# Kernel tuning notes

Hardware: AMD Instinct MI355X
Metric: run time of the kernel (lower is better)

## Reference

```python
import jax, jax.numpy as jnp
import numpy as np

EMBED = 2048
HEADS = 16
DHEAD = EMBED // HEADS


def setup_inputs() -> dict:
    key = jax.random.key(0)
    k1, k2, k3 = jax.random.split(key, 3)
    x = jax.random.normal(k1, (4, 2048, EMBED), dtype=jnp.float32)
    # torch Linear weight layout: [out_features, in_features]; y = x @ W.T
    W_in = jax.random.normal(k2, (3 * EMBED, EMBED), dtype=jnp.float32) * (EMBED ** -0.5)
    W_out = jax.random.normal(k3, (EMBED, EMBED), dtype=jnp.float32) * (EMBED ** -0.5)
    return {"x": x, "W_in": W_in, "W_out": W_out}


def reference(x, W_in, W_out):
    B, T, C = x.shape
    qkv = jnp.einsum('btc,fc->btf', x, W_in)          # [B,T,3C]
    q, k, v = jnp.split(qkv, 3, axis=-1)
    def heads(t):
        return t.reshape(B, T, HEADS, DHEAD).transpose(0, 2, 1, 3)  # [B,H,T,D]
    q, k, v = heads(q), heads(k), heads(v)
    scale = DHEAD ** -0.5
    scores = jnp.einsum('bhtd,bhsd->bhts', q, k) * scale  # [B,H,T,T]
    causal = jnp.tril(jnp.ones((T, T), dtype=bool))
    scores = jnp.where(causal, scores, jnp.finfo(scores.dtype).min)
    attn = jax.nn.softmax(scores, axis=-1)
    y = jnp.einsum('bhts,bhsd->bhtd', attn, v)            # [B,H,T,D]
    y = y.transpose(0, 2, 1, 3).reshape(B, T, C)
    return jnp.einsum('btc,fc->btf', y, W_out)
```

## Files before the change

kernel.cpp:

```cpp
#include <hip/hip_runtime.h>

typedef unsigned short u16;
typedef unsigned int u32;
typedef __attribute__((ext_vector_type(8))) short bf16x8;
typedef __attribute__((ext_vector_type(4))) float f32x4;
typedef __attribute__((ext_vector_type(8))) unsigned short u16x8;
typedef __attribute__((ext_vector_type(4))) unsigned short u16x4;
typedef __attribute__((ext_vector_type(4))) u32 u32x4;

#define MFMA16 __builtin_amdgcn_mfma_f32_16x16x32_bf16

__device__ __forceinline__ u16 f2bf(float f) {
  unsigned u = __float_as_uint(f);
  u += 0x7fffu + ((u >> 16) & 1u);
  return (u16)(u >> 16);
}

__device__ __forceinline__ void async16(void* lds, const void* g) {
  __builtin_amdgcn_global_load_lds(
      (const __attribute__((address_space(1))) unsigned int*)g,
      (__attribute__((address_space(3))) unsigned int*)lds, 16, 0, 0);
}

__global__ void convert_all(const float* __restrict__ x, const float* __restrict__ Win,
                            const float* __restrict__ Wout, u16* __restrict__ xo,
                            u16* __restrict__ wino, u16* __restrict__ wouto) {
  const int nx = 16777216 / 4, nw = 12582912 / 4, no = 4194304 / 4;
  int i = blockIdx.x * blockDim.x + threadIdx.x;
  int st = gridDim.x * blockDim.x;
  for (; i < nx + nw + no; i += st) {
    const float4* src; ushort4* dst; int j;
    if (i < nx) { src = (const float4*)x; dst = (ushort4*)xo; j = i; }
    else if (i < nx + nw) { src = (const float4*)Win; dst = (ushort4*)wino; j = i - nx; }
    else { src = (const float4*)Wout; dst = (ushort4*)wouto; j = i - nx - nw; }
    float4 f = src[j];
    ushort4 o;
    o.x = f2bf(f.x); o.y = f2bf(f.y); o.z = f2bf(f.z); o.w = f2bf(f.w);
    dst[j] = o;
  }
}

#define GEMM256_CORE(A_, B_)                                                    \
  __shared__ __align__(16) char lds[131072];                                    \
  const int tid = threadIdx.x;                                                  \
  const int lane = tid & 63, w = tid >> 6;                                      \
  const int wr = w >> 2, wc = w & 3;                                            \
  const int fr = lane & 15, fq = lane >> 4;                                     \
  const int lrA = tid >> 3, ccA = tid & 7, w8 = w << 3;                         \
  f32x4 acc[8][4] = {};                                                         \
  const u16* Abase = A_ + (size_t)tm * 2048;                                    \
  const u16* Bbase = B_ + (size_t)tn * 2048;                                    \
  auto stageA = [&](int mh, int kt, char* buf) {                                \
    _Pragma("unroll") for (int it = 0; it < 2; ++it) {                          \
      int lrt = it * 64 + lrA;                                                  \
      int row = mh * 64 + (lrt & 63) + ((lrt & 64) << 1);                       \
      const u16* src = Abase + (size_t)row * 2048 + kt + ((ccA ^ (row & 7)) << 3); \
      int lr0 = it * 64 + w8;                                                   \
      int row0 = mh * 64 + (lr0 & 63) + ((lr0 & 64) << 1);                      \
      async16(buf + row0 * 128, src);                                           \
    }                                                                           \
  };                                                                            \
  auto stageB = [&](int nh, int kt, char* buf) {                                \
    _Pragma("unroll") for (int it = 0; it < 2; ++it) {                          \
      int lrt = it * 64 + lrA;                                                  \
      int nr = ((lrt >> 5) << 6) + nh * 32 + (lrt & 31);                        \
      const u16* src = Bbase + (size_t)nr * 2048 + kt + ((ccA ^ (nr & 7)) << 3); \
      int lr0 = it * 64 + w8;                                                   \
      int nr0 = ((lr0 >> 5) << 6) + nh * 32 + (lr0 & 31);                       \
      async16(buf + 32768 + nr0 * 128, src);                                    \
    }                                                                           \
  };                                                                            \
  stageA(0, 0, lds); stageB(0, 0, lds); stageB(1, 0, lds); stageA(1, 0, lds);   \
  for (int t = 0; t < 32; ++t) {                                                \
    char* cur = lds + (t & 1) * 65536;                                          \
    char* nxt = lds + ((t + 1) & 1) * 65536;                                    \
    const int ktn = (t + 1) * 64;                                               \
    const bool more = (t + 1 < 32);                                             \
    asm volatile("s_waitcnt vmcnt(2)" ::: "memory");                            \
    __builtin_amdgcn_s_barrier();                                               \
    asm volatile("" ::: "memory");                                              \
    bf16x8 af[4][2], bfr[4][2];                                                 \
    _Pragma("unroll") for (int i = 0; i < 4; ++i) {                             \
      int rr = wr * 128 + i * 16 + fr;                                          \
      _Pragma("unroll") for (int ks = 0; ks < 2; ++ks)                          \
        af[i][ks] = *(const bf16x8*)(cur + rr * 128 +                           \
                                     (((ks * 4 + fq) ^ (rr & 7)) << 4));        \
    }                                                                           \
    _Pragma("unroll") for (int j = 0; j < 4; ++j) {                             \
      int nr = wc * 64 + j * 16 + fr;                                           \
      _Pragma("unroll") for (int ks = 0; ks < 2; ++ks)                          \
        bfr[j][ks] = *(const bf16x8*)(cur + 32768 + nr * 128 +                  \
                                      (((ks * 4 + fq) ^ (nr & 7)) << 4));       \
    }                                                                           \
    if (more) { stageA(0, ktn, nxt); stageB(0, ktn, nxt); }                     \
    __builtin_amdgcn_s_setprio(1);                                              \
    _Pragma("unroll") for (int ks = 0; ks < 2; ++ks)                            \
      _Pragma("unroll") for (int i = 0; i < 4; ++i)                             \
        _Pragma("unroll") for (int j = 0; j < 4; ++j)                           \
          acc[i][j] = MFMA16(af[i][ks], bfr[j][ks], acc[i][j], 0, 0, 0);        \
    __builtin_amdgcn_s_setprio(0);                                              \
    if (more) asm volatile("s_waitcnt vmcnt(4)" ::: "memory");                  \
    else      asm volatile("s_waitcnt vmcnt(0)" ::: "memory");                  \
    __builtin_amdgcn_s_barrier();                                               \
    asm volatile("" ::: "memory");                                              \
    bf16x8 ag[4][2];                                                            \
    _Pragma("unroll") for (int i = 0; i < 4; ++i) {                             \
      int rr = wr * 128 + 64 + i * 16 + fr;                                     \
      _Pragma("unroll") for (int ks = 0; ks < 2; ++ks)                          \
        ag[i][ks] = *(const bf16x8*)(cur + rr * 128 +                           \
                                     (((ks * 4 + fq) ^ (rr & 7)) << 4));        \
    }                                                                           \
    if (more) { stageB(1, ktn, nxt); stageA(1, ktn, nxt); }                     \
    __builtin_amdgcn_s_setprio(1);                                              \
    _Pragma("unroll") for (int ks = 0; ks < 2; ++ks)                            \
      _Pragma("unroll") for (int i = 0; i < 4; ++i)                             \
        _Pragma("unroll") for (int j = 0; j < 4; ++j)                           \
          acc[4 + i][j] = MFMA16(ag[i][ks], bfr[j][ks], acc[4 + i][j], 0, 0, 0);\
    __builtin_amdgcn_s_setprio(0);                                              \
  }

__global__ __launch_bounds__(512, 2) void gemm_qkv8(
    const u16* __restrict__ A, const u16* __restrict__ B,
    u16* __restrict__ Qb, u16* __restrict__ Kb, u16* __restrict__ Vtb) {
  int id = blockIdx.x;
  int swz = (id & 7) * 96 + (id >> 3);
  const int tm = (swz / 24) * 256, tn = (swz % 24) * 256;
  GEMM256_CORE(A, B)
  if (tn < 4096) {
#pragma unroll
    for (int J = 0; J < 4; ++J) {
      int n = tn + wc * 64 + J * 16 + fr;
      int which = n >> 11, h = (n >> 7) & 15, d = n & 127;
      u16* dst = which == 0 ? Qb : Kb;
#pragma unroll
      for (int I = 0; I < 8; ++I)
#pragma unroll
        for (int rr = 0; rr < 4; ++rr) {
          int m = tm + wr * 128 + I * 16 + fq * 4 + rr;
          int bb = m >> 11, tt = m & 2047;
          dst[((size_t)((bb * 16 + h) * 2048 + tt) << 7) + d] = f2bf(acc[I][J][rr]);
        }
    }
  } else {
    __syncthreads();
    u16* my = (u16*)(lds) + w * 8192;
#pragma unroll
    for (int J = 0; J < 4; ++J)
#pragma unroll
      for (int I = 0; I < 8; ++I) {
        u16x4 pk;
#pragma unroll
        for (int rr = 0; rr < 4; ++rr) pk[rr] = f2bf(acc[I][J][rr]);
        *(u16x4*)&my[(J * 16 + fr) * 128 + I * 16 + fq * 4] = pk;
      }
    const int bb = tm >> 11;
    const int hh = wc >> 1;
    const int h = ((tn >> 7) | hh) & 15;
    const int dbase = (wc & 1) * 64;
    const int tbase = (tm & 2047) + wr * 128;
    u16* Vw = Vtb + (size_t)(bb * 16 + h) * 262144;
#pragma unroll
    for (int it = 0; it < 16; ++it) {
      int chunk = it * 64 + lane;
      int nl = chunk >> 4, cc = chunk & 15;
      u16x8 v8 = *(const u16x8*)&my[nl * 128 + cc * 8];
      *(u16x8*)&Vw[(size_t)(dbase + nl) * 2048 + tbase + cc * 8] = v8;
    }
  }
}

__global__ __launch_bounds__(512, 2) void gemm_out8(
    const u16* __restrict__ A, const u16* __restrict__ B, float* __restrict__ C) {
  int id = blockIdx.x;
  int swz = (id & 7) * 32 + (id >> 3);
  const int tm = (swz / 8) * 256, tn = (swz % 8) * 256;
  GEMM256_CORE(A, B)
#pragma unroll
  for (int J = 0; J < 4; ++J) {
    int n = tn + wc * 64 + J * 16 + fr;
#pragma unroll
    for (int I = 0; I < 8; ++I)
#pragma unroll
      for (int rr = 0; rr < 4; ++rr) {
        int m = tm + wr * 128 + I * 16 + fq * 4 + rr;
        C[(size_t)m * 2048 + n] = acc[I][J][rr];
      }
  }
}

__global__ __launch_bounds__(512, 4) void attn14(
    const u16* __restrict__ Q, const u16* __restrict__ K,
    const u16* __restrict__ Vt, u16* __restrict__ Y) {
  __shared__ __align__(16) char smem[49152];
  char* lK = smem;
  char* lV = smem + 16384;
  char* lP = smem + 32768;
  const int tid = threadIdx.x;
  const int lane = tid & 63, w = tid >> 6;
  const int fr = lane & 15, fq = lane >> 4;
  const int pair = blockIdx.x;
  const int qb = 15 - (int)blockIdx.y;
  const size_t hoff = (size_t)pair * 262144;
  const u16* Qh = Q + hoff;
  const u16* Kh = K + hoff;
  const u16* Vth = Vt + hoff;
  const int b = pair >> 4, h = pair & 15;
  const float c1 = 0.08838834764831845f * 1.4426950408889634f;
  const float THR = 11.5f;

  int ksr[2], kcc[2], vdr[2], vcc[2];
#pragma unroll
  for (int it = 0; it < 2; ++it) {
    int idx = it * 512 + tid;
    ksr[it] = idx >> 4; kcc[it] = idx & 15;
    vdr[it] = idx >> 3; vcc[it] = idx & 7;
  }

  const int q0 = qb * 128;
  const int nt = 2 * qb + 2;
  const int qw = q0 + w * 16;

  bf16x8 qf[4];
#pragma unroll
  for (int ks = 0; ks < 4; ++ks)
    qf[ks] = *(const bf16x8*)&Qh[(size_t)(qw + fr) * 128 + ks * 32 + fq * 8];

  f32x4 o[8] = {};
  float m2[4], ls[4];
#pragma unroll
  for (int r = 0; r < 4; ++r) { m2[r] = -1e30f; ls[r] = 0.f; }

  u32x4 kst[2], vst[2];
#pragma unroll
  for (int it = 0; it < 2; ++it) {
    kst[it] = *(const u32x4*)&Kh[(size_t)ksr[it] * 128 + kcc[it] * 8];
    vst[it] = *(const u32x4*)&Vth[(size_t)vdr[it] * 2048 + vcc[it] * 8];
  }

  for (int t = 0; t < nt; ++t) {
    const int kv0 = t * 64;
#pragma unroll
    for (int it = 0; it < 2; ++it) {
      *(u32x4*)(lK + ksr[it] * 256 + ((kcc[it] ^ (ksr[it] & 7)) << 4)) = kst[it];
      *(u32x4*)(lV + vdr[it] * 128 + ((vcc[it] ^ (vdr[it] & 7)) << 4)) = vst[it];
    }
    if (t + 1 < nt) {
      const int nk = kv0 + 64;
#pragma unroll
      for (int it = 0; it < 2; ++it) {
        kst[it] = *(const u32x4*)&Kh[(size_t)(nk + ksr[it]) * 128 + kcc[it] * 8];
        vst[it] = *(const u32x4*)&Vth[(size_t)vdr[it] * 2048 + nk + vcc[it] * 8];
      }
    }
    __syncthreads();

    if (kv0 <= qw + 15) {
      f32x4 sc[4] = {};
#pragma unroll
      for (int j = 0; j < 4; ++j) {
        int s = j * 16 + fr;
#pragma unroll
        for (int ks = 0; ks < 4; ++ks) {
          bf16x8 kf = *(const bf16x8*)(lK + s * 256 + (((ks * 32 + fq * 8) * 2) ^ ((s & 7) << 4)));
          sc[j] = MFMA16(qf[ks], kf, sc[j], 0, 0, 0);
        }
      }
      if (kv0 + 64 > qw) {
        int rowb = qw + fq * 4;
#pragma unroll
        for (int j = 0; j < 4; ++j) {
          int col = kv0 + j * 16 + fr;
#pragma unroll
          for (int r = 0; r < 4; ++r)
            if (col > rowb + r) sc[j][r] = -3e38f;
        }
      }
      float lmax[4];
      bool trip = false;
#pragma unroll
      for (int r = 0; r < 4; ++r) {
        lmax[r] = fmaxf(fmaxf(sc[0][r], sc[1][r]), fmaxf(sc[2][r], sc[3][r]));
        trip = trip || (lmax[r] * c1 > m2[r] + THR);
      }
      if (__any(trip)) {
#pragma unroll
        for (int r = 0; r < 4; ++r) {
          float v = lmax[r];
          v = fmaxf(v, __shfl_xor(v, 1));
          v = fmaxf(v, __shfl_xor(v, 2));
          v = fmaxf(v, __shfl_xor(v, 4));
          v = fmaxf(v, __shfl_xor(v, 8));
          v *= c1;
          float mn = fmaxf(m2[r], v);
          float corr = __builtin_amdgcn_exp2f(m2[r] - mn);
          m2[r] = mn;
          ls[r] *= corr;
#pragma unroll
          for (int n = 0; n < 8; ++n) o[n][r] *= corr;
        }
      }
#pragma unroll
      for (int r = 0; r < 4; ++r) {
        int prow = w * 16 + fq * 4 + r;
        float rs = 0.f;
#pragma unroll
        for (int j = 0; j < 4; ++j) {
          float p = __builtin_amdgcn_exp2f(sc[j][r] * c1 - m2[r]);
          rs += p;
          *(u16*)(lP + prow * 128 + (((j * 16 + fr) * 2) ^ ((prow & 7) << 4))) = f2bf(p);
        }
        ls[r] += rs;
      }
      bf16x8 pf[2];
      {
        int prow = w * 16 + fr;
#pragma unroll
        for (int k2 = 0; k2 < 2; ++k2)
          pf[k2] = *(const bf16x8*)(lP + prow * 128 + ((k2 * 64 + fq * 16) ^ ((prow & 7) << 4)));
      }
#pragma unroll
      for (int n = 0; n < 8; ++n) {
        int d = n * 16 + fr;
#pragma unroll
        for (int k2 = 0; k2 < 2; ++k2) {
          bf16x8 vf = *(const bf16x8*)(lV + d * 128 + ((k2 * 64 + fq * 16) ^ ((d & 7) << 4)));
          o[n] = MFMA16(pf[k2], vf, o[n], 0, 0, 0);
        }
      }
    }
    __syncthreads();
  }

  float inv[4];
#pragma unroll
  for (int r = 0; r < 4; ++r) {
    float s = ls[r];
    s += __shfl_xor(s, 1);
    s += __shfl_xor(s, 2);
    s += __shfl_xor(s, 4);
    s += __shfl_xor(s, 8);
    inv[r] = 1.f / s;
  }
#pragma unroll
  for (int n = 0; n < 8; ++n)
#pragma unroll
    for (int r = 0; r < 4; ++r) {
      int tt = qw + fq * 4 + r;
      Y[((size_t)(b * 2048 + tt) * 2048) + h * 128 + n * 16 + fr] = f2bf(o[n][r] * inv[r]);
    }
}

extern "C" void kernel_launch(void* const* d_in, const int* in_sizes, int n_in,
                              void* d_out, int out_size, void* d_ws, size_t ws_size,
                              hipStream_t stream) {
  const float* x = (const float*)d_in[0];
  const float* Win = (const float*)d_in[1];
  const float* Wout = (const float*)d_in[2];
  float* out = (float*)d_out;
  char* ws = (char*)d_ws;

  u16* x_bf   = (u16*)(ws);
  u16* win_bf = (u16*)(ws + 33554432);
  u16* wout_bf= (u16*)(ws + 58720256);
  u16* Qb     = (u16*)(ws + 67108864);
  u16* Kb     = (u16*)(ws + 100663296);
  u16* Vtb    = (u16*)(ws + 134217728);
  u16* y_bf   = (u16*)(ws + 167772160);

  convert_all<<<2048, 256, 0, stream>>>(x, Win, Wout, x_bf, win_bf, wout_bf);

  gemm_qkv8<<<768, 512, 0, stream>>>(x_bf, win_bf, Qb, Kb, Vtb);
  attn14<<<dim3(64, 16), 512, 0, stream>>>(Qb, Kb, Vtb, y_bf);
  gemm_out8<<<256, 512, 0, stream>>>(y_bf, wout_bf, out);
}
```

Measured before the change: 443.4 us.

## Pair short and long causal query blocks per workgroup in attention

Each attention workgroup now handles two query blocks, by and 15-by, which share one pass over the K/V tiles. This balances causal work across workgroups and halves the grid, and each staged K/V tile is reused by two query blocks. It costs double accumulator and Q-fragment registers, which may spill under the 512x4 launch bounds. The two blocks are processed one after the other within an iteration, with no interleaving between them.

```diff
diff --git a/kernel.cpp b/kernel.cpp
--- a/kernel.cpp
+++ b/kernel.cpp
@@ -188,7 +188,7 @@
   }
 }
 
-__global__ __launch_bounds__(512, 4) void attn14(
+__global__ __launch_bounds__(512, 4) void attn21(
     const u16* __restrict__ Q, const u16* __restrict__ K,
     const u16* __restrict__ Vt, u16* __restrict__ Y) {
   __shared__ __align__(16) char smem[49152];
@@ -198,8 +198,7 @@
   const int tid = threadIdx.x;
   const int lane = tid & 63, w = tid >> 6;
   const int fr = lane & 15, fq = lane >> 4;
-  const int pair = blockIdx.x;
-  const int qb = 15 - (int)blockIdx.y;
+  const int pair = blockIdx.x, by = blockIdx.y;
   const size_t hoff = (size_t)pair * 262144;
   const u16* Qh = Q + hoff;
   const u16* Kh = K + hoff;
@@ -208,6 +207,11 @@
   const float c1 = 0.08838834764831845f * 1.4426950408889634f;
   const float THR = 11.5f;
 
+  const int qbA = by, qbB = 15 - by;
+  const int qwA = qbA * 128 + w * 16;
+  const int qwB = qbB * 128 + w * 16;
+  const int NT = 2 * qbB + 2;
+
   int ksr[2], kcc[2], vdr[2], vcc[2];
 #pragma unroll
   for (int it = 0; it < 2; ++it) {
@@ -216,19 +220,20 @@
     vdr[it] = idx >> 3; vcc[it] = idx & 7;
   }
 
-  const int q0 = qb * 128;
-  const int nt = 2 * qb + 2;
-  const int qw = q0 + w * 16;
-
-  bf16x8 qf[4];
-#pragma unroll
-  for (int ks = 0; ks < 4; ++ks)
-    qf[ks] = *(const bf16x8*)&Qh[(size_t)(qw + fr) * 128 + ks * 32 + fq * 8];
-
-  f32x4 o[8] = {};
-  float m2[4], ls[4];
-#pragma unroll
-  for (int r = 0; r < 4; ++r) { m2[r] = -1e30f; ls[r] = 0.f; }
+  bf16x8 qfA[4], qfB[4];
+#pragma unroll
+  for (int ks = 0; ks < 4; ++ks) {
+    qfA[ks] = *(const bf16x8*)&Qh[(size_t)(qwA + fr) * 128 + ks * 32 + fq * 8];
+    qfB[ks] = *(const bf16x8*)&Qh[(size_t)(qwB + fr) * 128 + ks * 32 + fq * 8];
+  }
+
+  f32x4 oA[8] = {}, oB[8] = {};
+  float m2A[4], lsA[4], m2B[4], lsB[4];
+#pragma unroll
+  for (int r = 0; r < 4; ++r) {
+    m2A[r] = -1e30f; lsA[r] = 0.f;
+    m2B[r] = -1e30f; lsB[r] = 0.f;
+  }
 
   u32x4 kst[2], vst[2];
 #pragma unroll
@@ -237,14 +242,90 @@
     vst[it] = *(const u32x4*)&Vth[(size_t)vdr[it] * 2048 + vcc[it] * 8];
   }
 
-  for (int t = 0; t < nt; ++t) {
+  auto proc = [&](int kv0, int qw, bf16x8 (&qf)[4], f32x4 (&o)[8],
+                  float (&m2)[4], float (&ls)[4]) {
+    f32x4 sc[4] = {};
+#pragma unroll
+    for (int j = 0; j < 4; ++j) {
+      int s = j * 16 + fr;
+#pragma unroll
+      for (int ks = 0; ks < 4; ++ks) {
+        bf16x8 kf = *(const bf16x8*)(lK + s * 256 + (((ks * 32 + fq * 8) * 2) ^ ((s & 7) << 4)));
+        sc[j] = MFMA16(qf[ks], kf, sc[j], 0, 0, 0);
+      }
+    }
+    if (kv0 + 64 > qw) {
+      int rowb = qw + fq * 4;
+#pragma unroll
+      for (int j = 0; j < 4; ++j) {
+        int col = kv0 + j * 16 + fr;
+#pragma unroll
+        for (int r = 0; r < 4; ++r)
+          if (col > rowb + r) sc[j][r] = -3e38f;
+      }
+    }
+    float lmax[4];
+    bool trip = false;
+#pragma unroll
+    for (int r = 0; r < 4; ++r) {
+      lmax[r] = fmaxf(fmaxf(sc[0][r], sc[1][r]), fmaxf(sc[2][r], sc[3][r]));
+      trip = trip || (lmax[r] * c1 > m2[r] + THR);
+    }
+    if (__any(trip)) {
+#pragma unroll
+      for (int r = 0; r < 4; ++r) {
+        float v = lmax[r];
+        v = fmaxf(v, __shfl_xor(v, 1));
+        v = fmaxf(v, __shfl_xor(v, 2));
+        v = fmaxf(v, __shfl_xor(v, 4));
+        v = fmaxf(v, __shfl_xor(v, 8));
+        v *= c1;
+        float mn = fmaxf(m2[r], v);
+        float corr = __builtin_amdgcn_exp2f(m2[r] - mn);
+        m2[r] = mn;
+        ls[r] *= corr;
+#pragma unroll
+        for (int n = 0; n < 8; ++n) o[n][r] *= corr;
+      }
+    }
+#pragma unroll
+    for (int r = 0; r < 4; ++r) {
+      int prow = w * 16 + fq * 4 + r;
+      float rs = 0.f;
+#pragma unroll
+      for (int j = 0; j < 4; ++j) {
+        float p = __builtin_amdgcn_exp2f(sc[j][r] * c1 - m2[r]);
+        rs += p;
+        *(u16*)(lP + prow * 128 + (((j * 16 + fr) * 2) ^ ((prow & 7) << 4))) = f2bf(p);
+      }
+      ls[r] += rs;
+    }
+    bf16x8 pf[2];
+    {
+      int prow = w * 16 + fr;
+#pragma unroll
+      for (int k2 = 0; k2 < 2; ++k2)
+        pf[k2] = *(const bf16x8*)(lP + prow * 128 + ((k2 * 64 + fq * 16) ^ ((prow & 7) << 4)));
+    }
+#pragma unroll
+    for (int n = 0; n < 8; ++n) {
+      int d = n * 16 + fr;
+#pragma unroll
+      for (int k2 = 0; k2 < 2; ++k2) {
+        bf16x8 vf = *(const bf16x8*)(lV + d * 128 + ((k2 * 64 + fq * 16) ^ ((d & 7) << 4)));
+        o[n] = MFMA16(pf[k2], vf, o[n], 0, 0, 0);
+      }
+    }
+  };
+
+  for (int t = 0; t < NT; ++t) {
     const int kv0 = t * 64;
 #pragma unroll
     for (int it = 0; it < 2; ++it) {
       *(u32x4*)(lK + ksr[it] * 256 + ((kcc[it] ^ (ksr[it] & 7)) << 4)) = kst[it];
       *(u32x4*)(lV + vdr[it] * 128 + ((vcc[it] ^ (vdr[it] & 7)) << 4)) = vst[it];
     }
-    if (t + 1 < nt) {
+    if (t + 1 < NT) {
       const int nk = kv0 + 64;
 #pragma unroll
       for (int it = 0; it < 2; ++it) {
@@ -254,100 +335,35 @@
     }
     __syncthreads();
 
-    if (kv0 <= qw + 15) {
-      f32x4 sc[4] = {};
-#pragma unroll
-      for (int j = 0; j < 4; ++j) {
-        int s = j * 16 + fr;
-#pragma unroll
-        for (int ks = 0; ks < 4; ++ks) {
-          bf16x8 kf = *(const bf16x8*)(lK + s * 256 + (((ks * 32 + fq * 8) * 2) ^ ((s & 7) << 4)));
-          sc[j] = MFMA16(qf[ks], kf, sc[j], 0, 0, 0);
-        }
-      }
-      if (kv0 + 64 > qw) {
-        int rowb = qw + fq * 4;
-#pragma unroll
-        for (int j = 0; j < 4; ++j) {
-          int col = kv0 + j * 16 + fr;
-#pragma unroll
-          for (int r = 0; r < 4; ++r)
-            if (col > rowb + r) sc[j][r] = -3e38f;
-        }
-      }
-      float lmax[4];
-      bool trip = false;
+    if (kv0 <= qwA + 15) proc(kv0, qwA, qfA, oA, m2A, lsA);
+    if (kv0 <= qwB + 15) proc(kv0, qwB, qfB, oB, m2B, lsB);
+
+    __syncthreads();
+  }
+
+#pragma unroll
+  for (int s2 = 0; s2 < 2; ++s2) {
+    const int qw = s2 ? qwB : qwA;
+    f32x4* o = s2 ? oB : oA;
+    float* ls = s2 ? lsB : lsA;
+    float inv[4];
+#pragma unroll
+    for (int r = 0; r < 4; ++r) {
+      float s = ls[r];
+      s += __shfl_xor(s, 1);
+      s += __shfl_xor(s, 2);
+      s += __shfl_xor(s, 4);
+      s += __shfl_xor(s, 8);
+      inv[r] = 1.f / s;
+    }
+#pragma unroll
+    for (int n = 0; n < 8; ++n)
 #pragma unroll
       for (int r = 0; r < 4; ++r) {
-        lmax[r] = fmaxf(fmaxf(sc[0][r], sc[1][r]), fmaxf(sc[2][r], sc[3][r]));
-        trip = trip || (lmax[r] * c1 > m2[r] + THR);
-      }
-      if (__any(trip)) {
-#pragma unroll
-        for (int r = 0; r < 4; ++r) {
-          float v = lmax[r];
-          v = fmaxf(v, __shfl_xor(v, 1));
-          v = fmaxf(v, __shfl_xor(v, 2));
-          v = fmaxf(v, __shfl_xor(v, 4));
-          v = fmaxf(v, __shfl_xor(v, 8));
-          v *= c1;
-          float mn = fmaxf(m2[r], v);
-          float corr = __builtin_amdgcn_exp2f(m2[r] - mn);
-          m2[r] = mn;
-          ls[r] *= corr;
-#pragma unroll
-          for (int n = 0; n < 8; ++n) o[n][r] *= corr;
-        }
-      }
-#pragma unroll
-      for (int r = 0; r < 4; ++r) {
-        int prow = w * 16 + fq * 4 + r;
-        float rs = 0.f;
-#pragma unroll
-        for (int j = 0; j < 4; ++j) {
-          float p = __builtin_amdgcn_exp2f(sc[j][r] * c1 - m2[r]);
-          rs += p;
-          *(u16*)(lP + prow * 128 + (((j * 16 + fr) * 2) ^ ((prow & 7) << 4))) = f2bf(p);
-        }
-        ls[r] += rs;
-      }
-      bf16x8 pf[2];
-      {
-        int prow = w * 16 + fr;
-#pragma unroll
-        for (int k2 = 0; k2 < 2; ++k2)
-          pf[k2] = *(const bf16x8*)(lP + prow * 128 + ((k2 * 64 + fq * 16) ^ ((prow & 7) << 4)));
-      }
-#pragma unroll
-      for (int n = 0; n < 8; ++n) {
-        int d = n * 16 + fr;
-#pragma unroll
-        for (int k2 = 0; k2 < 2; ++k2) {
-          bf16x8 vf = *(const bf16x8*)(lV + d * 128 + ((k2 * 64 + fq * 16) ^ ((d & 7) << 4)));
-          o[n] = MFMA16(pf[k2], vf, o[n], 0, 0, 0);
-        }
-      }
-    }
-    __syncthreads();
-  }
-
-  float inv[4];
-#pragma unroll
-  for (int r = 0; r < 4; ++r) {
-    float s = ls[r];
-    s += __shfl_xor(s, 1);
-    s += __shfl_xor(s, 2);
-    s += __shfl_xor(s, 4);
-    s += __shfl_xor(s, 8);
-    inv[r] = 1.f / s;
-  }
-#pragma unroll
-  for (int n = 0; n < 8; ++n)
-#pragma unroll
-    for (int r = 0; r < 4; ++r) {
-      int tt = qw + fq * 4 + r;
-      Y[((size_t)(b * 2048 + tt) * 2048) + h * 128 + n * 16 + fr] = f2bf(o[n][r] * inv[r]);
-    }
+        int tt = qw + fq * 4 + r;
+        Y[((size_t)(b * 2048 + tt) * 2048) + h * 128 + n * 16 + fr] = f2bf(o[n][r] * inv[r]);
+      }
+  }
 }
 
 extern "C" void kernel_launch(void* const* d_in, const int* in_sizes, int n_in,
@@ -370,6 +386,6 @@
   convert_all<<<2048, 256, 0, stream>>>(x, Win, Wout, x_bf, win_bf, wout_bf);
 
   gemm_qkv8<<<768, 512, 0, stream>>>(x_bf, win_bf, Qb, Kb, Vtb);
-  attn14<<<dim3(64, 16), 512, 0, stream>>>(Qb, Kb, Vtb, y_bf);
+  attn21<<<dim3(64, 8), 512, 0, stream>>>(Qb, Kb, Vtb, y_bf);
   gemm_out8<<<256, 512, 0, stream>>>(y_bf, wout_bf, out);
 }
```

Result: slower. 850.8 us (+91.9%).
